# Performance work log

Hardware: AMD Instinct MI355X
Metric: run time of the kernel (lower is better)

The kernel has to match this reference:

```python
import jax, jax.numpy as jnp
import numpy as np

B_SZ = 2
D_MODEL = 1024
H = 16
C = 8
BLK = 128
DK = 64
DV = 64
NCHUNK = 1024            # tokens per chunk (divisible by BLK)
T = C * (1 + NCHUNK)     # 8200: [g0, chunk0..., g1, chunk1..., ...]


def setup_inputs() -> dict:
    key = jax.random.key(0)
    k0, k1, k2, k3, k4 = jax.random.split(key, 5)
    s = 0.02
    x  = jax.random.normal(k0, (B_SZ, T, D_MODEL), dtype=jnp.float32)
    Wq = jax.random.normal(k1, (D_MODEL, H * DK), dtype=jnp.float32) * s
    Wk = jax.random.normal(k2, (D_MODEL, H * DK), dtype=jnp.float32) * s
    Wv = jax.random.normal(k3, (D_MODEL, H * DV), dtype=jnp.float32) * s
    Wo = jax.random.normal(k4, (H * DV, D_MODEL), dtype=jnp.float32) * s
    bo = jnp.zeros((D_MODEL,), dtype=jnp.float32)
    return {"x": x, "Wq": Wq, "Wk": Wk, "Wv": Wv, "Wo": Wo, "bo": bo}


def _local_sparse_3block(qf, kf, vf):
    # qf,kf: [BC, H, N, dk], vf: [BC, H, N, dv]; window = [left, current, right] blocks
    bc, h, n, dk = qf.shape
    dv = vf.shape[-1]
    nb = n // BLK
    q = qf.reshape(bc, h, nb, BLK, dk)
    k = kf.reshape(bc, h, nb, BLK, dk)
    v = vf.reshape(bc, h, nb, BLK, dv)
    zk = jnp.zeros((bc, h, 1, BLK, dk), qf.dtype)
    zv = jnp.zeros((bc, h, 1, BLK, dv), qf.dtype)
    kp = jnp.concatenate([zk, k, zk], axis=2)          # [bc,h,nb+2,B,dk]
    vp = jnp.concatenate([zv, v, zv], axis=2)
    k_win = jnp.concatenate([kp[:, :, 0:nb], kp[:, :, 1:nb + 1], kp[:, :, 2:nb + 2]], axis=3)  # [bc,h,nb,3B,dk]
    v_win = jnp.concatenate([vp[:, :, 0:nb], vp[:, :, 1:nb + 1], vp[:, :, 2:nb + 2]], axis=3)  # [bc,h,nb,3B,dv]
    scale = 1.0 / np.sqrt(dk).astype(np.float32)
    scores = jnp.einsum('bhnqd,bhnkd->bhnqk', q, k_win) * scale   # [bc,h,nb,B,3B]
    mask = np.zeros((nb, 3 * BLK), dtype=bool)
    mask[0, :BLK] = True           # first block: left padding invalid
    mask[-1, 2 * BLK:] = True      # last block: right padding invalid
    scores = jnp.where(jnp.asarray(mask)[None, None, :, None, :], -jnp.inf, scores)
    attn = jax.nn.softmax(scores, axis=-1)
    out = jnp.einsum('bhnqk,bhnkd->bhnqd', attn, v_win)
    return out.reshape(bc, h, n, dv)


def reference(x, Wq, Wk, Wv, Wo, bo):
    Bb, Tt, _ = x.shape
    q = (x @ Wq).reshape(Bb, Tt, H, DK).transpose(0, 2, 1, 3)  # [B,H,T,dk]
    k = (x @ Wk).reshape(Bb, Tt, H, DK).transpose(0, 2, 1, 3)
    v = (x @ Wv).reshape(Bb, Tt, H, DV).transpose(0, 2, 1, 3)
    stride = NCHUNK + 1
    g_idx = jnp.arange(C) * stride
    gq = q[:, :, g_idx]  # [B,H,C,dk]
    gk = k[:, :, g_idx]
    gv = v[:, :, g_idx]  # [B,H,C,dv]
    local_idx = ((g_idx + 1)[:, None] + jnp.arange(NCHUNK)[None, :]).reshape(-1)
    qx = q[:, :, local_idx].reshape(Bb, H, C, NCHUNK, DK)
    kx = k[:, :, local_idx].reshape(Bb, H, C, NCHUNK, DK)
    vx = v[:, :, local_idx].reshape(Bb, H, C, NCHUNK, DV)
    # local 3-block attention per chunk
    q_flat = qx.transpose(0, 2, 1, 3, 4).reshape(Bb * C, H, NCHUNK, DK)
    k_flat = kx.transpose(0, 2, 1, 3, 4).reshape(Bb * C, H, NCHUNK, DK)
    v_flat = vx.transpose(0, 2, 1, 3, 4).reshape(Bb * C, H, NCHUNK, DV)
    out_local = _local_sparse_3block(q_flat, k_flat, v_flat)
    out_local = out_local.reshape(Bb, C, H, NCHUNK, DV).transpose(0, 2, 1, 3, 4)  # [B,H,C,Nchunk,dv]
    # each local token additionally receives its chunk's global value directly
    out_chunks = out_local + gv[:, :, :, None, :]
    # global tokens attend over all globals + own chunk's locals (joint softmax, fp32)
    scale = 1.0 / np.sqrt(DK).astype(np.float32)
    scores_gg = jnp.einsum('bhcd,bhed->bhce', gq, gk) * scale      # [B,H,C,C]
    scores_gl = jnp.einsum('bhcd,bhcnd->bhcn', gq, kx) * scale     # [B,H,C,Nchunk]
    attn = jax.nn.softmax(jnp.concatenate([scores_gg, scores_gl], axis=-1), axis=-1)
    a_gg, a_gl = attn[..., :C], attn[..., C:]
    out_g = (jnp.einsum('bhce,bhed->bhcd', a_gg, gv)
             + jnp.einsum('bhcn,bhcnd->bhcd', a_gl, vx))           # [B,H,C,dv]
    out_inter = jnp.concatenate([out_g[:, :, :, None, :], out_chunks], axis=3)  # [B,H,C,1+Nchunk,dv]
    out = out_inter.reshape(Bb, H, Tt, DV).transpose(0, 2, 1, 3).reshape(Bb, Tt, H * DV)
    return out @ Wo + bo
```

## Files before the change

### kernel.cpp

```cpp
#include <hip/hip_runtime.h>
#include <hip/hip_bf16.h>

typedef __bf16 bf16x8 __attribute__((ext_vector_type(8)));
typedef float  f32x4  __attribute__((ext_vector_type(4)));
typedef unsigned short u16x8 __attribute__((ext_vector_type(8)));
typedef unsigned short u16x4 __attribute__((ext_vector_type(4)));

#define T_TOK   8200
#define M_TOK   16400
#define QKV_LD  3072
#define DM      1024

#define AS1CU const __attribute__((address_space(1))) unsigned int*
#define AS3U  __attribute__((address_space(3))) unsigned int*
#define GLDS16(g, s) __builtin_amdgcn_global_load_lds((AS1CU)(g), (AS3U)(s), 16, 0, 0)

__device__ __forceinline__ unsigned short f2bf(float f){
  __hip_bfloat16 h = __float2bfloat16(f);
  return *reinterpret_cast<unsigned short*>(&h);
}
__device__ __forceinline__ float bf2f(unsigned short u){
  union { unsigned u; float f; } x; x.u = ((unsigned)u) << 16;
  return x.f;
}

__global__ void k_cvt(const float* __restrict__ in, unsigned short* __restrict__ out, long n4){
  long i = (long)blockIdx.x * blockDim.x + threadIdx.x;
  long stride = (long)gridDim.x * blockDim.x;
  for (long e = i; e < n4; e += stride){
    float4 v = ((const float4*)in)[e];
    u16x4 o; o[0]=f2bf(v.x); o[1]=f2bf(v.y); o[2]=f2bf(v.z); o[3]=f2bf(v.w);
    ((u16x4*)out)[e] = o;
  }
}

__global__ __launch_bounds__(256) void k_wT4(const float* __restrict__ Wq, const float* __restrict__ Wk,
                                             const float* __restrict__ Wv, const float* __restrict__ Wo,
                                             unsigned short* __restrict__ wqkvt, unsigned short* __restrict__ wot){
  __shared__ float t[64][65];
  const float* W; unsigned short* Wt;
  int z = blockIdx.z;
  if      (z == 0){ W = Wq; Wt = wqkvt; }
  else if (z == 1){ W = Wk; Wt = wqkvt + (size_t)1024*1024; }
  else if (z == 2){ W = Wv; Wt = wqkvt + (size_t)2048*1024; }
  else            { W = Wo; Wt = wot; }
  int tk0 = blockIdx.x * 64, tn0 = blockIdx.y * 64;
  int tid = threadIdx.x;
#pragma unroll
  for (int i = 0; i < 4; i++){
    int ch = tid + i*256; int kr = ch >> 4, n4 = (ch & 15) * 4;
    float4 v = *(const float4*)(W + (size_t)(tk0+kr)*1024 + tn0 + n4);
    t[kr][n4+0]=v.x; t[kr][n4+1]=v.y; t[kr][n4+2]=v.z; t[kr][n4+3]=v.w;
  }
  __syncthreads();
#pragma unroll
  for (int i = 0; i < 4; i++){
    int ch = tid + i*256; int nr = ch >> 4, k4 = (ch & 15) * 4;
    u16x4 o;
#pragma unroll
    for (int e = 0; e < 4; e++) o[e] = f2bf(t[k4+e][nr]);
    *(u16x4*)(Wt + (size_t)(tn0+nr)*1024 + tk0 + k4) = o;
  }
}

__global__ __launch_bounds__(256,2) void k_gemm(const unsigned short* __restrict__ A,
                                                const unsigned short* __restrict__ Bt,
                                                const float* __restrict__ bias,
                                                void* __restrict__ Cout,
                                                int M, int K, int ldc, int bf16out, int gn){
  __shared__ unsigned short As[128][64];
  __shared__ unsigned short Bs[128][64];
  int tid = threadIdx.x, l = tid & 63, w = tid >> 6;
  int li = l & 15, lh = l >> 4;
  int nwg = gridDim.x;
  int wg = (blockIdx.x & 7) * (nwg >> 3) + (blockIdx.x >> 3);
  int m0 = (wg / gn) * 128, n0 = (wg % gn) * 128;
  int wm = (w & 1) * 64, wn = (w >> 1) * 64;
  int lr = l >> 3, lc = l & 7;
  int lsw = li & 7;

  f32x4 acc[4][4];
#pragma unroll
  for (int a = 0; a < 4; a++)
#pragma unroll
    for (int b = 0; b < 4; b++) acc[a][b] = 0.f;

  for (int kt = 0; kt < K; kt += 64){
    __syncthreads();
#pragma unroll
    for (int i = 0; i < 4; i++){
      int r = w*32 + i*8 + lr;
      int colsw = (lc ^ (r & 7)) * 8;
      int rga = m0 + r; if (rga >= M) rga = M - 1;
      GLDS16(A  + (size_t)rga     *K + kt + colsw, &As[w*32 + i*8][0]);
      GLDS16(Bt + (size_t)(n0 + r)*K + kt + colsw, &Bs[w*32 + i*8][0]);
    }
    __syncthreads();
#pragma unroll
    for (int ks = 0; ks < 2; ks++){
      bf16x8 af[4], bfr[4];
#pragma unroll
      for (int mt = 0; mt < 4; mt++)
        af[mt] = *(const bf16x8*)&As[wm + mt*16 + li][((ks*4 + lh) ^ lsw) * 8];
#pragma unroll
      for (int nt = 0; nt < 4; nt++)
        bfr[nt] = *(const bf16x8*)&Bs[wn + nt*16 + li][((ks*4 + lh) ^ lsw) * 8];
#pragma unroll
      for (int mt = 0; mt < 4; mt++)
#pragma unroll
        for (int nt = 0; nt < 4; nt++)
          acc[mt][nt] = __builtin_amdgcn_mfma_f32_16x16x32_bf16(af[mt], bfr[nt], acc[mt][nt], 0, 0, 0);
    }
  }
#pragma unroll
  for (int mt = 0; mt < 4; mt++)
#pragma unroll
    for (int nt = 0; nt < 4; nt++)
#pragma unroll
      for (int r = 0; r < 4; r++){
        int row = m0 + wm + mt*16 + lh*4 + r;
        int col = n0 + wn + nt*16 + li;
        if (row < M){
          float v = acc[mt][nt][r] + (bias ? bias[col] : 0.f);
          if (bf16out) ((unsigned short*)Cout)[(size_t)row*ldc + col] = f2bf(v);
          else         ((float*)Cout)[(size_t)row*ldc + col] = v;
        }
      }
}

__global__ __launch_bounds__(256,3) void k_local(const unsigned short* __restrict__ qkv,
                                                 unsigned short* __restrict__ att){
  __shared__ unsigned short Ks[128][64];
  __shared__ unsigned short Vt[64][136];
  __shared__ unsigned short PbV[9216];

  int tid = threadIdx.x, l = tid & 63, w = tid >> 6;
  int li = l & 15, lh = l >> 4;
  int lr = l >> 3, lc = l & 7;
  int lsw = li & 7;
  int wg = (blockIdx.x & 7) * 256 + (blockIdx.x >> 3);
  int blk = wg & 7, c = (wg >> 3) & 7, h = (wg >> 6) & 15, b = wg >> 10;
  size_t bT = (size_t)b * T_TOK;
  int tokq0 = c*1025 + 1 + blk*128;

  bf16x8 aq[2][2];
#pragma unroll
  for (int tr = 0; tr < 2; tr++)
#pragma unroll
    for (int ks = 0; ks < 2; ks++)
      aq[tr][ks] = *(const bf16x8*)(qkv + (bT + tokq0 + w*32 + tr*16 + li)*QKV_LD + h*64 + ks*32 + lh*8);

  float mrun[2][4], lrun[2][4];
  f32x4 oacc[2][4];
#pragma unroll
  for (int tr = 0; tr < 2; tr++)
#pragma unroll
    for (int r = 0; r < 4; r++){ mrun[tr][r] = -3e38f; lrun[tr][r] = 0.f; }
#pragma unroll
  for (int tr = 0; tr < 2; tr++)
#pragma unroll
    for (int ct = 0; ct < 4; ct++) oacc[tr][ct] = 0.f;

  for (int kb = blk-1; kb <= blk+1; ++kb){
    if ((unsigned)kb > 7u) continue;
    int tokk0 = c*1025 + 1 + kb*128;
    __syncthreads();
#pragma unroll
    for (int i = 0; i < 4; i++){
      int r = w*32 + i*8 + lr;
      int colk = (lc ^ (r & 7)) * 8;
      GLDS16(qkv + (bT + tokk0 + r)*QKV_LD + 1024 + h*64 + colk, &Ks[w*32 + i*8][0]);
    }
#pragma unroll
    for (int i = 0; i < 4; i++){
      int ch = tid + i*256; int r = ch >> 3, g = ch & 7;
      u16x8 vv = *(const u16x8*)(qkv + (bT + tokk0 + r)*QKV_LD + 2048 + h*64 + g*8);
      int gs = g ^ ((r >> 3) & 7);
      *(u16x8*)&PbV[r*72 + gs*8] = vv;
    }
    __syncthreads();
#pragma unroll
    for (int dd = 0; dd < 16; dd++){
      int d = w*16 + dd; int gd = d >> 3, dl = d & 7;
      int r0 = 2*l;
      int gsw = (gd ^ ((r0 >> 3) & 7)) * 8 + dl;
      unsigned lo = PbV[ r0   *72 + gsw];
      unsigned hi = PbV[(r0+1)*72 + gsw];
      *(unsigned*)&Vt[d][2*l] = lo | (hi << 16);
    }
    __syncthreads();

    f32x4 s2[2][8];
#pragma unroll
    for (int tr = 0; tr < 2; tr++)
#pragma unroll
      for (int ct = 0; ct < 8; ct++) s2[tr][ct] = 0.f;
#pragma unroll
    for (int ct = 0; ct < 8; ct++)
#pragma unroll
      for (int ks = 0; ks < 2; ks++){
        bf16x8 kf = *(const bf16x8*)&Ks[ct*16 + li][((ks*4 + lh) ^ lsw) * 8];
        s2[0][ct] = __builtin_amdgcn_mfma_f32_16x16x32_bf16(aq[0][ks], kf, s2[0][ct], 0, 0, 0);
        s2[1][ct] = __builtin_amdgcn_mfma_f32_16x16x32_bf16(aq[1][ks], kf, s2[1][ct], 0, 0, 0);
      }

    for (int tr = 0; tr < 2; tr++){
      float rmax[4] = {-3e38f,-3e38f,-3e38f,-3e38f};
#pragma unroll
      for (int ct = 0; ct < 8; ct++)
#pragma unroll
        for (int r = 0; r < 4; r++){
          float v = s2[tr][ct][r] * 0.125f; s2[tr][ct][r] = v;
          rmax[r] = fmaxf(rmax[r], v);
        }
#pragma unroll
      for (int r = 0; r < 4; r++)
#pragma unroll
        for (int mk = 1; mk < 16; mk <<= 1)
          rmax[r] = fmaxf(rmax[r], __shfl_xor(rmax[r], mk));
      float alpha[4], rsum[4] = {0.f,0.f,0.f,0.f};
#pragma unroll
      for (int r = 0; r < 4; r++){
        float mn = fmaxf(mrun[tr][r], rmax[r]);
        alpha[r] = __expf(mrun[tr][r] - mn);
        mrun[tr][r] = mn;
      }
#pragma unroll
      for (int ct = 0; ct < 8; ct++)
#pragma unroll
        for (int r = 0; r < 4; r++){
          float p = __expf(s2[tr][ct][r] - mrun[tr][r]);
          s2[tr][ct][r] = p; rsum[r] += p;
        }
#pragma unroll
      for (int r = 0; r < 4; r++)
#pragma unroll
        for (int mk = 1; mk < 16; mk <<= 1)
          rsum[r] += __shfl_xor(rsum[r], mk);
#pragma unroll
      for (int r = 0; r < 4; r++) lrun[tr][r] = lrun[tr][r]*alpha[r] + rsum[r];
#pragma unroll
      for (int ct = 0; ct < 4; ct++)
#pragma unroll
        for (int r = 0; r < 4; r++) oacc[tr][ct][r] *= alpha[r];
#pragma unroll
      for (int ct = 0; ct < 8; ct++)
#pragma unroll
        for (int r = 0; r < 4; r++)
          PbV[w*2176 + (lh*4 + r)*136 + ct*16 + li] = f2bf(s2[tr][ct][r]);
      bf16x8 pa[4];
#pragma unroll
      for (int ks = 0; ks < 4; ks++)
        pa[ks] = *(const bf16x8*)&PbV[w*2176 + li*136 + ks*32 + lh*8];
#pragma unroll
      for (int ct = 0; ct < 4; ct++)
#pragma unroll
        for (int ks = 0; ks < 4; ks++){
          bf16x8 vfr = *(const bf16x8*)&Vt[ct*16 + li][ks*32 + lh*8];
          oacc[tr][ct] = __builtin_amdgcn_mfma_f32_16x16x32_bf16(pa[ks], vfr, oacc[tr][ct], 0, 0, 0);
        }
    }
  }

  float gvv[4];
#pragma unroll
  for (int ct = 0; ct < 4; ct++)
    gvv[ct] = bf2f(qkv[(bT + c*1025)*QKV_LD + 2048 + h*64 + ct*16 + li]);
#pragma unroll
  for (int tr = 0; tr < 2; tr++)
#pragma unroll
    for (int ct = 0; ct < 4; ct++)
#pragma unroll
      for (int r = 0; r < 4; r++){
        int row = w*32 + tr*16 + lh*4 + r;
        float v = oacc[tr][ct][r] / lrun[tr][r] + gvv[ct];
        att[(bT + tokq0 + row)*DM + h*64 + ct*16 + li] = f2bf(v);
      }
}

__global__ __launch_bounds__(256) void k_global(const unsigned short* __restrict__ qkv,
                                                unsigned short* __restrict__ att){
  __shared__ float sc[1032];
  __shared__ float red[256];
  __shared__ float gq_s[64];
  int tid = threadIdx.x, bid = blockIdx.x;
  int c = bid & 7, h = (bid >> 3) & 15, b = bid >> 7;
  size_t bT = (size_t)b * T_TOK;
  size_t grow = bT + (size_t)c*1025;
  if (tid < 64) gq_s[tid] = bf2f(qkv[grow*QKV_LD + h*64 + tid]);
  __syncthreads();
  float lmax = -3e38f;
  for (int idx = tid; idx < 1032; idx += 256){
    size_t krow = (idx < 8) ? (bT + (size_t)idx*1025) : (bT + (size_t)c*1025 + 1 + (idx - 8));
    const unsigned short* kp = qkv + krow*QKV_LD + 1024 + h*64;
    float s = 0.f;
#pragma unroll
    for (int d0 = 0; d0 < 64; d0 += 8){
      u16x8 kv = *(const u16x8*)(kp + d0);
#pragma unroll
      for (int e = 0; e < 8; e++) s += gq_s[d0+e] * bf2f(kv[e]);
    }
    s *= 0.125f;
    sc[idx] = s;
    lmax = fmaxf(lmax, s);
  }
  red[tid] = lmax; __syncthreads();
  for (int st = 128; st > 0; st >>= 1){ if (tid < st) red[tid] = fmaxf(red[tid], red[tid+st]); __syncthreads(); }
  float m = red[0]; __syncthreads();
  float lsum = 0.f;
  for (int idx = tid; idx < 1032; idx += 256){
    float p = __expf(sc[idx] - m); sc[idx] = p; lsum += p;
  }
  red[tid] = lsum; __syncthreads();
  for (int st = 128; st > 0; st >>= 1){ if (tid < st) red[tid] += red[tid+st]; __syncthreads(); }
  float denom = red[0]; __syncthreads();
  int d = tid & 63, part = tid >> 6;
  float acc = 0.f;
  for (int idx = part; idx < 1032; idx += 4){
    size_t krow = (idx < 8) ? (bT + (size_t)idx*1025) : (bT + (size_t)c*1025 + 1 + (idx - 8));
    acc += sc[idx] * bf2f(qkv[krow*QKV_LD + 2048 + h*64 + d]);
  }
  red[tid] = acc; __syncthreads();
  if (tid < 64){
    float o = (red[tid] + red[tid+64] + red[tid+128] + red[tid+192]) / denom;
    att[grow*DM + h*64 + tid] = f2bf(o);
  }
}

extern "C" void kernel_launch(void* const* d_in, const int* in_sizes, int n_in,
                              void* d_out, int out_size, void* d_ws, size_t ws_size,
                              hipStream_t stream) {
  const float* x  = (const float*)d_in[0];
  const float* Wq = (const float*)d_in[1];
  const float* Wk = (const float*)d_in[2];
  const float* Wv = (const float*)d_in[3];
  const float* Wo = (const float*)d_in[4];
  const float* bo = (const float*)d_in[5];
  float* out = (float*)d_out;

  unsigned short* xb    = (unsigned short*)d_ws;
  unsigned short* wqkvt = xb    + (size_t)M_TOK * 1024;
  unsigned short* wot   = wqkvt + (size_t)3072 * 1024;
  unsigned short* qkv   = wot   + (size_t)1024 * 1024;
  unsigned short* att   = qkv   + (size_t)M_TOK * QKV_LD;

  long n4 = (long)M_TOK * 1024 / 4;
  k_cvt<<<2048, 256, 0, stream>>>(x, xb, n4);
  k_wT4<<<dim3(16,16,4), 256, 0, stream>>>(Wq, Wk, Wv, Wo, wqkvt, wot);
  k_gemm<<<dim3(129*24), 256, 0, stream>>>(xb, wqkvt, (const float*)nullptr, (void*)qkv,
                                           M_TOK, 1024, QKV_LD, 1, 24);
  k_local<<<2048, 256, 0, stream>>>(qkv, att);
  k_global<<<256, 256, 0, stream>>>(qkv, att);
  k_gemm<<<dim3(129*8), 256, 0, stream>>>(att, wot, bo, (void*)out,
                                          M_TOK, 1024, DM, 0, 8);
}
```

Before: 370.8 us.

## Simplify V transpose in local attention and split QKV GEMM launch in two

The local attention kernel now issues its V global loads into registers before the barrier and scatters them straight into a transposed LDS tile padded to 138 columns. This removes the intermediate staging buffer pass and one __syncthreads per key block. The P buffer becomes its own [4][16][136] array. Separately, the QKV projection GEMM is launched as two grids covering the first 65 and the remaining 64 row tiles, which adds a launch and splits the wave across two kernels.

```diff
diff --git a/kernel.cpp b/kernel.cpp
--- a/kernel.cpp
+++ b/kernel.cpp
@@ -131,8 +131,8 @@
 __global__ __launch_bounds__(256,3) void k_local(const unsigned short* __restrict__ qkv,
                                                  unsigned short* __restrict__ att){
   __shared__ unsigned short Ks[128][64];
-  __shared__ unsigned short Vt[64][136];
-  __shared__ unsigned short PbV[9216];
+  __shared__ unsigned short Vt[64][138];
+  __shared__ unsigned short Pb[4][16][136];
 
   int tid = threadIdx.x, l = tid & 63, w = tid >> 6;
   int li = l & 15, lh = l >> 4;
@@ -164,6 +164,14 @@
   for (int kb = blk-1; kb <= blk+1; ++kb){
     if ((unsigned)kb > 7u) continue;
     int tokk0 = c*1025 + 1 + kb*128;
+
+    u16x8 vv[4];
+    int rr[4], gg[4];
+#pragma unroll
+    for (int i = 0; i < 4; i++){
+      int ch = tid + i*256; rr[i] = ch >> 3; gg[i] = ch & 7;
+      vv[i] = *(const u16x8*)(qkv + (bT + tokk0 + rr[i])*QKV_LD + 2048 + h*64 + gg[i]*8);
+    }
     __syncthreads();
 #pragma unroll
     for (int i = 0; i < 4; i++){
@@ -172,22 +180,10 @@
       GLDS16(qkv + (bT + tokk0 + r)*QKV_LD + 1024 + h*64 + colk, &Ks[w*32 + i*8][0]);
     }
 #pragma unroll
-    for (int i = 0; i < 4; i++){
-      int ch = tid + i*256; int r = ch >> 3, g = ch & 7;
-      u16x8 vv = *(const u16x8*)(qkv + (bT + tokk0 + r)*QKV_LD + 2048 + h*64 + g*8);
-      int gs = g ^ ((r >> 3) & 7);
-      *(u16x8*)&PbV[r*72 + gs*8] = vv;
-    }
-    __syncthreads();
-#pragma unroll
-    for (int dd = 0; dd < 16; dd++){
-      int d = w*16 + dd; int gd = d >> 3, dl = d & 7;
-      int r0 = 2*l;
-      int gsw = (gd ^ ((r0 >> 3) & 7)) * 8 + dl;
-      unsigned lo = PbV[ r0   *72 + gsw];
-      unsigned hi = PbV[(r0+1)*72 + gsw];
-      *(unsigned*)&Vt[d][2*l] = lo | (hi << 16);
-    }
+    for (int i = 0; i < 4; i++)
+#pragma unroll
+      for (int e = 0; e < 8; e++)
+        Vt[gg[i]*8 + e][rr[i]] = vv[i][e];
     __syncthreads();
 
     f32x4 s2[2][8];
@@ -247,11 +243,11 @@
       for (int ct = 0; ct < 8; ct++)
 #pragma unroll
         for (int r = 0; r < 4; r++)
-          PbV[w*2176 + (lh*4 + r)*136 + ct*16 + li] = f2bf(s2[tr][ct][r]);
+          Pb[w][lh*4 + r][ct*16 + li] = f2bf(s2[tr][ct][r]);
       bf16x8 pa[4];
 #pragma unroll
       for (int ks = 0; ks < 4; ks++)
-        pa[ks] = *(const bf16x8*)&PbV[w*2176 + li*136 + ks*32 + lh*8];
+        pa[ks] = *(const bf16x8*)&Pb[w][li][ks*32 + lh*8];
 #pragma unroll
       for (int ct = 0; ct < 4; ct++)
 #pragma unroll
@@ -347,8 +343,12 @@
   long n4 = (long)M_TOK * 1024 / 4;
   k_cvt<<<2048, 256, 0, stream>>>(x, xb, n4);
   k_wT4<<<dim3(16,16,4), 256, 0, stream>>>(Wq, Wk, Wv, Wo, wqkvt, wot);
-  k_gemm<<<dim3(129*24), 256, 0, stream>>>(xb, wqkvt, (const float*)nullptr, (void*)qkv,
-                                           M_TOK, 1024, QKV_LD, 1, 24);
+  const int MH = 65 * 128;
+  k_gemm<<<dim3(65*24), 256, 0, stream>>>(xb, wqkvt, (const float*)nullptr, (void*)qkv,
+                                          MH, 1024, QKV_LD, 1, 24);
+  k_gemm<<<dim3(64*24), 256, 0, stream>>>(xb + (size_t)MH*1024, wqkvt, (const float*)nullptr,
+                                          (void*)(qkv + (size_t)MH*QKV_LD),
+                                          M_TOK - MH, 1024, QKV_LD, 1, 24);
   k_local<<<2048, 256, 0, stream>>>(qkv, att);
   k_global<<<256, 256, 0, stream>>>(qkv, att);
   k_gemm<<<dim3(129*8), 256, 0, stream>>>(att, wot, bo, (void*)out,
```

New measurement: 374.4 us. About the same (+1.0%).
